# Performance work log

Hardware: AMD Instinct MI355X
Metric: run time of the kernel (lower is better)

The kernel has to match this reference:

```python
import jax, jax.numpy as jnp
import numpy as np


def setup_inputs() -> dict:
    key = jax.random.key(0)
    k1, k2 = jax.random.split(key)
    B, F = 512, 1024
    K, D = 100, 5
    inputs = jax.random.normal(k1, (B, F), dtype=jnp.float32)
    T = jax.random.normal(k2, (F, K * D), dtype=jnp.float32) * 0.05  # random_normal init
    return {"inputs": inputs, "T": T}


def reference(inputs, T):
    NUM_KERNELS, DIM_PER_KERNEL = 100, 5
    B = inputs.shape[0]
    # project: [B, F] @ [F, K*D] -> [B, K, D]
    x = (inputs @ T).reshape(B, NUM_KERNELS, DIM_PER_KERNEL)
    # pairwise L1 over D: abs_diffs[i, k, j] = sum_d |x[i,k,d] - x[j,k,d]|
    # diffs: [B, K, D, B]
    diffs = x[:, :, :, None] - jnp.transpose(x, (1, 2, 0))[None, :, :, :]
    abs_diffs = jnp.sum(jnp.abs(diffs), axis=2)  # [B, K, B]
    # sum over other-batch axis (includes self term exp(0)=1, as in original)
    minibatch_features = jnp.sum(jnp.exp(-abs_diffs), axis=2)  # [B, K]
    return minibatch_features
```

## Files before the change

kernel.cpp:

```cpp
#include <hip/hip_runtime.h>


#define BB 512
#define FF 1024
#define KK 100
#define KD 500
#define KDP 512
#define SPLITS 8
#define FN (FF / SPLITS)

__global__ __launch_bounds__(256, 2) void proj_tile(
    const float* __restrict__ in, const float* __restrict__ T,
    float* __restrict__ xp)
{
    const int i0  = blockIdx.x * 64;
    const int kd0 = blockIdx.y * 64;
    const int s   = blockIdx.z;
    const int t   = threadIdx.x;
    const int tk  = t & 15;
    const int ti  = t >> 4;

    __shared__ float Ads[16][68];
    __shared__ float Bds[16][64];

    float acc[4][4];
    #pragma unroll
    for (int r = 0; r < 4; ++r)
        #pragma unroll
        for (int c = 0; c < 4; ++c) acc[r][c] = 0.f;

    const int ia  = t >> 2;
    const int fqa = t & 3;
    const int kb  = t & 63;
    const int frb = t >> 6;
    const int kbc = min(kd0 + kb, KD - 1);

    for (int step = 0; step < FN / 16; ++step) {
        const int fs = s * FN + step * 16;
        __syncthreads();
        float4 av = *(const float4*)&in[(size_t)(i0 + ia) * FF + fs + fqa * 4];
        Ads[fqa * 4 + 0][ia] = av.x;
        Ads[fqa * 4 + 1][ia] = av.y;
        Ads[fqa * 4 + 2][ia] = av.z;
        Ads[fqa * 4 + 3][ia] = av.w;
        #pragma unroll
        for (int r = 0; r < 4; ++r)
            Bds[frb * 4 + r][kb] = T[(size_t)(fs + frb * 4 + r) * KD + kbc];
        __syncthreads();

        #pragma unroll
        for (int f = 0; f < 16; ++f) {
            float4 a = *(const float4*)&Ads[f][ti * 4];
            float4 b = *(const float4*)&Bds[f][tk * 4];
            float ar[4] = {a.x, a.y, a.z, a.w};
            float br[4] = {b.x, b.y, b.z, b.w};
            #pragma unroll
            for (int r = 0; r < 4; ++r)
                #pragma unroll
                for (int c = 0; c < 4; ++c)
                    acc[r][c] = fmaf(ar[r], br[c], acc[r][c]);
        }
    }

    #pragma unroll
    for (int r = 0; r < 4; ++r) {
        float4 v = {acc[r][0], acc[r][1], acc[r][2], acc[r][3]};
        *(float4*)&xp[((size_t)s * BB + i0 + ti * 4 + r) * KDP + kd0 + tk * 4] = v;
    }
}

__global__ __launch_bounds__(256) void reduce_x(
    const float* __restrict__ xp, float* __restrict__ x)
{
    const int e = blockIdx.x * 256 + threadIdx.x;
    const float4* xp4 = (const float4*)xp;
    float4 v = xp4[e];
    #pragma unroll
    for (int s = 1; s < SPLITS; ++s) {
        float4 w = xp4[(size_t)s * (BB * KDP / 4) + e];
        v.x += w.x; v.y += w.y; v.z += w.z; v.w += w.w;
    }
    ((float4*)x)[e] = v;
}

__global__ __launch_bounds__(512) void pair2k(
    const float* __restrict__ x, float* __restrict__ out)
{
    const int i0 = blockIdx.x * 64;
    const int kp = blockIdx.y;
    const int t  = threadIdx.x;
    const int lane = t & 63;
    const int w    = t >> 6;

    __shared__ float xs[BB][12];
    __shared__ float ps[8][64][2];

    const int kbase = kp * 10;
    #pragma unroll
    for (int it = 0; it < 5; ++it) {
        int e = t + it * 512;
        int j = e / 5;
        int c = e - j * 5;
        float2 f2 = *(const float2*)&x[(size_t)j * KDP + kbase + c * 2];
        *(float2*)&xs[j][c * 2] = f2;
    }
    __syncthreads();

    const int i = i0 + lane;
    const float4 xi0 = *(const float4*)&xs[i][0];
    const float4 xi1 = *(const float4*)&xs[i][4];
    const float2 xi2 = *(const float2*)&xs[i][8];
    const float NEG_LOG2E = -1.4426950408889634f;

    float s0 = 0.f, s1 = 0.f;
    #pragma unroll 4
    for (int jj = 0; jj < 64; ++jj) {
        const int j = (w << 6) + jj;
        float4 xj0 = *(const float4*)&xs[j][0];
        float4 xj1 = *(const float4*)&xs[j][4];
        float2 xj2 = *(const float2*)&xs[j][8];
        float aa0 = (fabsf(xi0.x - xj0.x) + fabsf(xi0.y - xj0.y))
                  + (fabsf(xi0.z - xj0.z) + fabsf(xi0.w - xj0.w))
                  + fabsf(xi1.x - xj1.x);
        float aa1 = (fabsf(xi1.y - xj1.y) + fabsf(xi1.z - xj1.z))
                  + (fabsf(xi1.w - xj1.w) + fabsf(xi2.x - xj2.x))
                  + fabsf(xi2.y - xj2.y);
        s0 += __builtin_amdgcn_exp2f(NEG_LOG2E * aa0);
        s1 += __builtin_amdgcn_exp2f(NEG_LOG2E * aa1);
    }

    ps[w][lane][0] = s0;
    ps[w][lane][1] = s1;
    __syncthreads();

    if (t < 128) {
        const int li = t & 63;
        const int kk = t >> 6;
        float v = 0.f;
        #pragma unroll
        for (int q = 0; q < 8; ++q) v += ps[q][li][kk];
        out[(size_t)(i0 + li) * KK + kp * 2 + kk] = v;
    }
}

__global__ __launch_bounds__(1024, 1) void mbd_fused(
    const float* __restrict__ in, const float* __restrict__ T, float* __restrict__ out)
{
    const int k = blockIdx.x;
    const int t = threadIdx.x;
    const int i = t & (BB - 1);
    const int h = t >> 9;

    __shared__ float xk[1024][8];

    float a0 = 0.f, a1 = 0.f, a2 = 0.f, a3 = 0.f, a4 = 0.f;
    const float4* inrow = (const float4*)(in + (size_t)i * FF + (size_t)h * 512);
    const float* Tk = T + 5 * k + (size_t)h * 512 * KD;

    for (int ff = 0; ff < 512; ff += 4) {
        float4 v = inrow[ff >> 2];
        const float* tp = Tk + (size_t)ff * KD;
        a0 = fmaf(v.x, tp[0], a0); a1 = fmaf(v.x, tp[1], a1); a2 = fmaf(v.x, tp[2], a2);
        a3 = fmaf(v.x, tp[3], a3); a4 = fmaf(v.x, tp[4], a4); tp += KD;
        a0 = fmaf(v.y, tp[0], a0); a1 = fmaf(v.y, tp[1], a1); a2 = fmaf(v.y, tp[2], a2);
        a3 = fmaf(v.y, tp[3], a3); a4 = fmaf(v.y, tp[4], a4); tp += KD;
        a0 = fmaf(v.z, tp[0], a0); a1 = fmaf(v.z, tp[1], a1); a2 = fmaf(v.z, tp[2], a2);
        a3 = fmaf(v.z, tp[3], a3); a4 = fmaf(v.z, tp[4], a4); tp += KD;
        a0 = fmaf(v.w, tp[0], a0); a1 = fmaf(v.w, tp[1], a1); a2 = fmaf(v.w, tp[2], a2);
        a3 = fmaf(v.w, tp[3], a3); a4 = fmaf(v.w, tp[4], a4);
    }
    xk[t][0] = a0; xk[t][1] = a1; xk[t][2] = a2; xk[t][3] = a3; xk[t][4] = a4;
    __syncthreads();
    if (t < BB) {
        xk[t][0] += xk[t + BB][0]; xk[t][1] += xk[t + BB][1]; xk[t][2] += xk[t + BB][2];
        xk[t][3] += xk[t + BB][3]; xk[t][4] += xk[t + BB][4];
    }
    __syncthreads();

    const int jg = t >> 9;
    const float4 xiv = *(const float4*)&xk[i][0];
    const float xi4 = xk[i][4];
    const float NEG_LOG2E = -1.4426950408889634f;
    float s0 = 0.f;
    const int j0 = jg << 8;
    for (int jj = 0; jj < 256; ++jj) {
        const int j = j0 + jj;
        float4 xj = *(const float4*)&xk[j][0];
        float xj4 = xk[j][4];
        float aa = (fabsf(xiv.x - xj.x) + fabsf(xiv.y - xj.y))
                 + (fabsf(xiv.z - xj.z) + fabsf(xiv.w - xj.w)) + fabsf(xi4 - xj4);
        s0 += __builtin_amdgcn_exp2f(NEG_LOG2E * aa);
    }
    xk[BB + i][jg] = s0;
    __syncthreads();
    if (t < BB)
        out[(size_t)t * KK + k] = xk[BB + t][0] + xk[BB + t][1];
}

extern "C" void kernel_launch(void* const* d_in, const int* in_sizes, int n_in,
                              void* d_out, int out_size, void* d_ws, size_t ws_size,
                              hipStream_t stream) {
    const float* in = (const float*)d_in[0];
    const float* T  = (const float*)d_in[1];
    float* out = (float*)d_out;

    const size_t xp_bytes = (size_t)SPLITS * BB * KDP * sizeof(float);
    const size_t x_bytes  = (size_t)BB * KDP * sizeof(float);

    if (ws_size < xp_bytes + x_bytes) {
        mbd_fused<<<KK, 1024, 0, stream>>>(in, T, out);
        return;
    }

    float* xp = (float*)d_ws;
    float* x  = (float*)((char*)d_ws + xp_bytes);

    dim3 g1(BB / 64, KDP / 64, SPLITS);
    proj_tile<<<g1, 256, 0, stream>>>(in, T, xp);

    reduce_x<<<(BB * KDP / 4) / 256, 256, 0, stream>>>(xp, x);

    dim3 g3(BB / 64, KK / 2);
    pair2k<<<g3, 512, 0, stream>>>(x, out);
}
```

Baseline: 37.81 us.

## Prefetch GEMM tiles, deepen K-split, transpose-reduce with prescale, coalesce pair loads

The projection GEMM now prefetches the next 16-wide A/B slices into registers while computing the current one. It also doubles the F-split count to 16 and raises the occupancy hint, to add parallelism and hide load latency. The reduction kernel now sums the partials, transposes them into a [KD][B] layout and prescales by log2(e). This lets the pairwise kernel load its slice with coalesced per-thread reads and drop a multiply before exp2. The pairwise loop also uses split accumulators for more ILP. In exchange, the partial-sum buffer doubles in size, which adds global write and read traffic. If the workspace is too small, the code falls back to the slow fused kernel.

```diff
diff --git a/kernel.cpp b/kernel.cpp
--- a/kernel.cpp
+++ b/kernel.cpp
@@ -6,10 +6,13 @@
 #define KK 100
 #define KD 500
 #define KDP 512
-#define SPLITS 8
+#define SPLITS 16
 #define FN (FF / SPLITS)
-
-__global__ __launch_bounds__(256, 2) void proj_tile(
+#define STEPS (FN / 16)
+
+#define LOG2E 1.4426950408889634f
+
+__global__ __launch_bounds__(256, 4) void proj_tile(
     const float* __restrict__ in, const float* __restrict__ T,
     float* __restrict__ xp)
 {
@@ -35,18 +38,34 @@
     const int frb = t >> 6;
     const int kbc = min(kd0 + kb, KD - 1);
 
-    for (int step = 0; step < FN / 16; ++step) {
-        const int fs = s * FN + step * 16;
-        __syncthreads();
-        float4 av = *(const float4*)&in[(size_t)(i0 + ia) * FF + fs + fqa * 4];
+    const float* inb = in + (size_t)(i0 + ia) * FF + s * FN;
+    const float* Tb  = T + (size_t)(s * FN) * KD + kbc;
+
+    float4 av = *(const float4*)&inb[fqa * 4];
+    float bv0 = Tb[(size_t)(frb * 4 + 0) * KD];
+    float bv1 = Tb[(size_t)(frb * 4 + 1) * KD];
+    float bv2 = Tb[(size_t)(frb * 4 + 2) * KD];
+    float bv3 = Tb[(size_t)(frb * 4 + 3) * KD];
+
+    for (int step = 0; step < STEPS; ++step) {
         Ads[fqa * 4 + 0][ia] = av.x;
         Ads[fqa * 4 + 1][ia] = av.y;
         Ads[fqa * 4 + 2][ia] = av.z;
         Ads[fqa * 4 + 3][ia] = av.w;
-        #pragma unroll
-        for (int r = 0; r < 4; ++r)
-            Bds[frb * 4 + r][kb] = T[(size_t)(fs + frb * 4 + r) * KD + kbc];
+        Bds[frb * 4 + 0][kb] = bv0;
+        Bds[frb * 4 + 1][kb] = bv1;
+        Bds[frb * 4 + 2][kb] = bv2;
+        Bds[frb * 4 + 3][kb] = bv3;
         __syncthreads();
+
+        if (step + 1 < STEPS) {
+            const int fo = (step + 1) * 16;
+            av  = *(const float4*)&inb[fo + fqa * 4];
+            bv0 = Tb[(size_t)(fo + frb * 4 + 0) * KD];
+            bv1 = Tb[(size_t)(fo + frb * 4 + 1) * KD];
+            bv2 = Tb[(size_t)(fo + frb * 4 + 2) * KD];
+            bv3 = Tb[(size_t)(fo + frb * 4 + 3) * KD];
+        }
 
         #pragma unroll
         for (int f = 0; f < 16; ++f) {
@@ -60,6 +79,7 @@
                 for (int c = 0; c < 4; ++c)
                     acc[r][c] = fmaf(ar[r], br[c], acc[r][c]);
         }
+        if (step + 1 < STEPS) __syncthreads();
     }
 
     #pragma unroll
@@ -69,22 +89,39 @@
     }
 }
 
-__global__ __launch_bounds__(256) void reduce_x(
-    const float* __restrict__ xp, float* __restrict__ x)
-{
-    const int e = blockIdx.x * 256 + threadIdx.x;
-    const float4* xp4 = (const float4*)xp;
-    float4 v = xp4[e];
-    #pragma unroll
-    for (int s = 1; s < SPLITS; ++s) {
-        float4 w = xp4[(size_t)s * (BB * KDP / 4) + e];
+__global__ __launch_bounds__(256) void reduce_t(
+    const float* __restrict__ xp, float* __restrict__ xT)
+{
+    const int kd0 = blockIdx.x * 32;
+    const int i0  = blockIdx.y * 32;
+    const int t   = threadIdx.x;
+    const int c4  = t & 7;
+    const int rr  = t >> 3;
+
+    __shared__ float tile[32][33];
+
+    const float4* p = (const float4*)xp + ((size_t)(i0 + rr) * KDP + kd0) / 4 + c4;
+    float4 v = {0.f, 0.f, 0.f, 0.f};
+    #pragma unroll
+    for (int s = 0; s < SPLITS; ++s) {
+        float4 w = p[(size_t)s * (BB * KDP / 4)];
         v.x += w.x; v.y += w.y; v.z += w.z; v.w += w.w;
     }
-    ((float4*)x)[e] = v;
+    tile[rr][c4 * 4 + 0] = v.x;
+    tile[rr][c4 * 4 + 1] = v.y;
+    tile[rr][c4 * 4 + 2] = v.z;
+    tile[rr][c4 * 4 + 3] = v.w;
+    __syncthreads();
+
+    float4 o = { tile[c4 * 4 + 0][rr] * LOG2E,
+                 tile[c4 * 4 + 1][rr] * LOG2E,
+                 tile[c4 * 4 + 2][rr] * LOG2E,
+                 tile[c4 * 4 + 3][rr] * LOG2E };
+    *(float4*)&xT[(size_t)(kd0 + rr) * BB + i0 + c4 * 4] = o;
 }
 
 __global__ __launch_bounds__(512) void pair2k(
-    const float* __restrict__ x, float* __restrict__ out)
+    const float* __restrict__ xT, float* __restrict__ out)
 {
     const int i0 = blockIdx.x * 64;
     const int kp = blockIdx.y;
@@ -97,40 +134,50 @@
 
     const int kbase = kp * 10;
     #pragma unroll
-    for (int it = 0; it < 5; ++it) {
-        int e = t + it * 512;
-        int j = e / 5;
-        int c = e - j * 5;
-        float2 f2 = *(const float2*)&x[(size_t)j * KDP + kbase + c * 2];
-        *(float2*)&xs[j][c * 2] = f2;
-    }
+    for (int c = 0; c < 10; ++c)
+        xs[t][c] = xT[(size_t)(kbase + c) * BB + t];
     __syncthreads();
 
     const int i = i0 + lane;
     const float4 xi0 = *(const float4*)&xs[i][0];
     const float4 xi1 = *(const float4*)&xs[i][4];
     const float2 xi2 = *(const float2*)&xs[i][8];
-    const float NEG_LOG2E = -1.4426950408889634f;
-
-    float s0 = 0.f, s1 = 0.f;
-    #pragma unroll 4
-    for (int jj = 0; jj < 64; ++jj) {
-        const int j = (w << 6) + jj;
-        float4 xj0 = *(const float4*)&xs[j][0];
-        float4 xj1 = *(const float4*)&xs[j][4];
-        float2 xj2 = *(const float2*)&xs[j][8];
-        float aa0 = (fabsf(xi0.x - xj0.x) + fabsf(xi0.y - xj0.y))
-                  + (fabsf(xi0.z - xj0.z) + fabsf(xi0.w - xj0.w))
-                  + fabsf(xi1.x - xj1.x);
-        float aa1 = (fabsf(xi1.y - xj1.y) + fabsf(xi1.z - xj1.z))
-                  + (fabsf(xi1.w - xj1.w) + fabsf(xi2.x - xj2.x))
-                  + fabsf(xi2.y - xj2.y);
-        s0 += __builtin_amdgcn_exp2f(NEG_LOG2E * aa0);
-        s1 += __builtin_amdgcn_exp2f(NEG_LOG2E * aa1);
-    }
-
-    ps[w][lane][0] = s0;
-    ps[w][lane][1] = s1;
+
+    float s00 = 0.f, s01 = 0.f, s10 = 0.f, s11 = 0.f;
+    #pragma unroll 2
+    for (int jj = 0; jj < 64; jj += 2) {
+        {
+            const int j = (w << 6) + jj;
+            float4 xj0 = *(const float4*)&xs[j][0];
+            float4 xj1 = *(const float4*)&xs[j][4];
+            float2 xj2 = *(const float2*)&xs[j][8];
+            float aa0 = (fabsf(xi0.x - xj0.x) + fabsf(xi0.y - xj0.y))
+                      + (fabsf(xi0.z - xj0.z) + fabsf(xi0.w - xj0.w))
+                      + fabsf(xi1.x - xj1.x);
+            float aa1 = (fabsf(xi1.y - xj1.y) + fabsf(xi1.z - xj1.z))
+                      + (fabsf(xi1.w - xj1.w) + fabsf(xi2.x - xj2.x))
+                      + fabsf(xi2.y - xj2.y);
+            s00 += __builtin_amdgcn_exp2f(-aa0);
+            s10 += __builtin_amdgcn_exp2f(-aa1);
+        }
+        {
+            const int j = (w << 6) + jj + 1;
+            float4 xj0 = *(const float4*)&xs[j][0];
+            float4 xj1 = *(const float4*)&xs[j][4];
+            float2 xj2 = *(const float2*)&xs[j][8];
+            float aa0 = (fabsf(xi0.x - xj0.x) + fabsf(xi0.y - xj0.y))
+                      + (fabsf(xi0.z - xj0.z) + fabsf(xi0.w - xj0.w))
+                      + fabsf(xi1.x - xj1.x);
+            float aa1 = (fabsf(xi1.y - xj1.y) + fabsf(xi1.z - xj1.z))
+                      + (fabsf(xi1.w - xj1.w) + fabsf(xi2.x - xj2.x))
+                      + fabsf(xi2.y - xj2.y);
+            s01 += __builtin_amdgcn_exp2f(-aa0);
+            s11 += __builtin_amdgcn_exp2f(-aa1);
+        }
+    }
+
+    ps[w][lane][0] = s00 + s01;
+    ps[w][lane][1] = s10 + s11;
     __syncthreads();
 
     if (t < 128) {
@@ -213,13 +260,14 @@
     }
 
     float* xp = (float*)d_ws;
-    float* x  = (float*)((char*)d_ws + xp_bytes);
+    float* xT = (float*)((char*)d_ws + xp_bytes);
 
     dim3 g1(BB / 64, KDP / 64, SPLITS);
     proj_tile<<<g1, 256, 0, stream>>>(in, T, xp);
 
-    reduce_x<<<(BB * KDP / 4) / 256, 256, 0, stream>>>(xp, x);
+    dim3 g2(KDP / 32, BB / 32);
+    reduce_t<<<g2, 256, 0, stream>>>(xp, xT);
 
     dim3 g3(BB / 64, KK / 2);
-    pair2k<<<g3, 512, 0, stream>>>(x, out);
-}
+    pair2k<<<g3, 512, 0, stream>>>(xT, out);
+}
```

Result: faster. 35.79 us (-5.3%).
